# Kernel optimization log

Hardware: AMD Instinct MI355X
Metric: run time of the kernel (lower is better)

The kernel has to match this reference:

```python
import jax, jax.numpy as jnp
import numpy as np

B, N, C, D = 1, 8192, 256, 128
MASK_VAL = jnp.float32(-1e16)


def setup_inputs() -> dict:
    key = jax.random.key(0)
    k_in, k_g, k_w, k_b = jax.random.split(key, 4)
    inputs = jax.random.normal(k_in, (B, N, C), dtype=jnp.float32)
    # row has at least one unmasked entry (standard GAT practice).
    graph = (jax.random.uniform(k_g, (N, N)) < 0.01).astype(jnp.float32)
    graph = jnp.maximum(graph, jnp.eye(N, dtype=jnp.float32))
    W = jax.random.normal(k_w, (D, C), dtype=jnp.float32)  # nn.Linear weight [out,in]
    b = jax.random.normal(k_b, (D,), dtype=jnp.float32)
    return {"inputs": inputs, "graph": graph, "W": W, "b": b}


def reference(inputs, graph, W, b):
    # h = W(inputs): [B,N,D]
    h = jnp.einsum('bnc,dc->bnd', inputs, W)
    # dense scores masked by adjacency: [B,N,N]
    scores = jnp.einsum('bnd,bmd->bnm', h, h) * graph[None, :, :]
    # torch: masked_fill_(scores == 0, -1e16)
    scores = jnp.where(scores == 0.0, MASK_VAL, scores)
    attention = jax.nn.softmax(scores, axis=2)
    return jnp.einsum('bnm,bmd->bnd', attention, h) + b
```

## Files before the change

### kernel.cpp

```cpp
#include <hip/hip_runtime.h>
#include <math.h>

#define Nn 8192
#define Cc 256
#define Dd 128
#define CAP 192

typedef float fx4 __attribute__((ext_vector_type(4)));

__global__ __launch_bounds__(256) void wt_kernel(const float* __restrict__ W,
                                                 float4* __restrict__ WT) {
  const int t = blockIdx.x * 256 + threadIdx.x;
  const int c4 = t >> 7;
  const int d  = t & 127;
  const float4 v = *(const float4*)(W + (size_t)d * Cc + c4 * 4);
  WT[c4 * Dd + d] = v;
}

__global__ __launch_bounds__(256) void h_kernel(const float* __restrict__ x,
                                                const float4* __restrict__ WT,
                                                float* __restrict__ h) {
  const int tid = threadIdx.x;
  const int d = tid & 127;
  const int g = tid >> 7;
  const int r0 = blockIdx.x * 16 + g * 8;
  const float4* x4 = (const float4*)(x + (size_t)r0 * Cc);

  float acc[8];
#pragma unroll
  for (int r = 0; r < 8; ++r) acc[r] = 0.f;

#pragma unroll 4
  for (int c4 = 0; c4 < Cc / 4; ++c4) {
    const float4 w = WT[c4 * Dd + d];
#pragma unroll
    for (int r = 0; r < 8; ++r) {
      const float4 u = x4[r * (Cc / 4) + c4];
      acc[r] += u.x * w.x + u.y * w.y + u.z * w.z + u.w * w.w;
    }
  }
#pragma unroll
  for (int r = 0; r < 8; ++r) {
    h[(size_t)(r0 + r) * Dd + d] = acc[r];
  }
}

__global__ __launch_bounds__(256) void gat_fused(const float* __restrict__ graph,
                                                 const float* __restrict__ h,
                                                 const float* __restrict__ bias,
                                                 float* __restrict__ out) {
  __shared__ int idxs[4][CAP];
  const int wv   = threadIdx.x >> 6;
  const int lane = threadIdx.x & 63;
  const int i = blockIdx.x * 4 + wv;
  int* idx = idxs[wv];

  const float2 hi2 = *(const float2*)(h + (size_t)i * Dd + lane * 2);

  const fx4* row = (const fx4*)(graph + (size_t)i * Nn);
  const unsigned long long lmask = (1ull << lane) - 1ull;
  int cnt = 0;

  fx4 v[8];
#pragma unroll
  for (int t = 0; t < 8; ++t)
    v[t] = __builtin_nontemporal_load(&row[t * 64 + lane]);

#pragma unroll
  for (int c = 0; c < 4; ++c) {
    fx4 nv[8];
    if (c < 3) {
#pragma unroll
      for (int t = 0; t < 8; ++t)
        nv[t] = __builtin_nontemporal_load(&row[(c + 1) * 8 * 64 + t * 64 + lane]);
    }
#pragma unroll
    for (int t = 0; t < 8; ++t) {
      const int col = 4 * ((c * 8 + t) * 64 + lane);
      {
        const unsigned long long mk = __ballot(v[t].x != 0.f);
        const int p = cnt + __popcll(mk & lmask);
        if (v[t].x != 0.f && p < CAP) idx[p] = col + 0;
        cnt += __popcll(mk);
      }
      {
        const unsigned long long mk = __ballot(v[t].y != 0.f);
        const int p = cnt + __popcll(mk & lmask);
        if (v[t].y != 0.f && p < CAP) idx[p] = col + 1;
        cnt += __popcll(mk);
      }
      {
        const unsigned long long mk = __ballot(v[t].z != 0.f);
        const int p = cnt + __popcll(mk & lmask);
        if (v[t].z != 0.f && p < CAP) idx[p] = col + 2;
        cnt += __popcll(mk);
      }
      {
        const unsigned long long mk = __ballot(v[t].w != 0.f);
        const int p = cnt + __popcll(mk & lmask);
        if (v[t].w != 0.f && p < CAP) idx[p] = col + 3;
        cnt += __popcll(mk);
      }
    }
#pragma unroll
    for (int t = 0; t < 8; ++t) v[t] = nv[t];
  }
  const int m = min(cnt, CAP);

  float M = -INFINITY, L = 0.f;
  float accx = 0.f, accy = 0.f;

  float2 hv[8];
#pragma unroll
  for (int t = 0; t < 8; ++t) {
    if (t < m) {
      const int j = idx[t];
      hv[t] = *(const float2*)(h + (size_t)j * Dd + lane * 2);
    }
  }

  for (int e0 = 0; e0 < m; e0 += 8) {
    const int ne = min(8, m - e0);
    const int rem = m - e0 - 8;
    float2 nhv[8];
#pragma unroll
    for (int t = 0; t < 8; ++t) {
      if (t < rem) {
        const int j = idx[e0 + 8 + t];
        nhv[t] = *(const float2*)(h + (size_t)j * Dd + lane * 2);
      }
    }
#pragma unroll
    for (int t = 0; t < 8; ++t) {
      if (t < ne) {
        float pd = hi2.x * hv[t].x + hi2.y * hv[t].y;
#pragma unroll
        for (int off = 32; off > 0; off >>= 1) pd += __shfl_xor(pd, off);
        const float s = pd;
        if (s != 0.f) {
          const float newM = fmaxf(M, s);
          const float scale = __expf(M - newM);
          const float p = __expf(s - newM);
          L = L * scale + p;
          accx = accx * scale + p * hv[t].x;
          accy = accy * scale + p * hv[t].y;
          M = newM;
        }
      }
    }
#pragma unroll
    for (int t = 0; t < 8; ++t) hv[t] = nhv[t];
  }

  const float inv = 1.f / L;
  const float2 bv = *(const float2*)(bias + lane * 2);
  float2 o;
  o.x = accx * inv + bv.x;
  o.y = accy * inv + bv.y;
  *(float2*)(out + (size_t)i * Dd + lane * 2) = o;
}

extern "C" void kernel_launch(void* const* d_in, const int* in_sizes, int n_in,
                              void* d_out, int out_size, void* d_ws, size_t ws_size,
                              hipStream_t stream) {
  const float* x     = (const float*)d_in[0];
  const float* graph = (const float*)d_in[1];
  const float* W     = (const float*)d_in[2];
  const float* bias  = (const float*)d_in[3];
  float* out = (float*)d_out;

  float*  h  = (float*)d_ws;
  float4* WT = (float4*)((char*)d_ws + (16u << 20));

  wt_kernel<<<32, 256, 0, stream>>>(W, WT);
  h_kernel<<<Nn / 16, 256, 0, stream>>>(x, WT, h);
  gat_fused<<<Nn / 4, 256, 0, stream>>>(graph, h, bias, out);
}
```

Measured before the change: 459.3 us.

## Split wavefront into four 16-lane groups processing neighbors in parallel

The neighbor aggregation phase now splits each 64-lane wavefront into four 16-lane quarters. Each quarter handles a different neighbor and each lane holds 8 feature elements. This cuts the dot-product shuffle reduction from 6 steps to 4 and processes four edges per step instead of one. Each quarter keeps its own online-softmax state, and the four states are merged with cross-quarter shuffles at the end. This adds merge overhead and more registers per lane.

```diff
diff --git a/kernel.cpp b/kernel.cpp
--- a/kernel.cpp
+++ b/kernel.cpp
@@ -52,10 +52,13 @@
   __shared__ int idxs[4][CAP];
   const int wv   = threadIdx.x >> 6;
   const int lane = threadIdx.x & 63;
+  const int q    = lane >> 4;
+  const int ql   = lane & 15;
   const int i = blockIdx.x * 4 + wv;
   int* idx = idxs[wv];
 
-  const float2 hi2 = *(const float2*)(h + (size_t)i * Dd + lane * 2);
+  const float4 hiA = *(const float4*)(h + (size_t)i * Dd + ql * 8);
+  const float4 hiB = *(const float4*)(h + (size_t)i * Dd + ql * 8 + 4);
 
   const fx4* row = (const fx4*)(graph + (size_t)i * Nn);
   const unsigned long long lmask = (1ull << lane) - 1ull;
@@ -108,56 +111,97 @@
   const int m = min(cnt, CAP);
 
   float M = -INFINITY, L = 0.f;
-  float accx = 0.f, accy = 0.f;
-
-  float2 hv[8];
-#pragma unroll
-  for (int t = 0; t < 8; ++t) {
-    if (t < m) {
-      const int j = idx[t];
-      hv[t] = *(const float2*)(h + (size_t)j * Dd + lane * 2);
-    }
-  }
-
-  for (int e0 = 0; e0 < m; e0 += 8) {
-    const int ne = min(8, m - e0);
-    const int rem = m - e0 - 8;
-    float2 nhv[8];
-#pragma unroll
-    for (int t = 0; t < 8; ++t) {
-      if (t < rem) {
-        const int j = idx[e0 + 8 + t];
-        nhv[t] = *(const float2*)(h + (size_t)j * Dd + lane * 2);
-      }
-    }
-#pragma unroll
-    for (int t = 0; t < 8; ++t) {
-      if (t < ne) {
-        float pd = hi2.x * hv[t].x + hi2.y * hv[t].y;
-#pragma unroll
-        for (int off = 32; off > 0; off >>= 1) pd += __shfl_xor(pd, off);
-        const float s = pd;
-        if (s != 0.f) {
-          const float newM = fmaxf(M, s);
-          const float scale = __expf(M - newM);
-          const float p = __expf(s - newM);
-          L = L * scale + p;
-          accx = accx * scale + p * hv[t].x;
-          accy = accy * scale + p * hv[t].y;
-          M = newM;
-        }
-      }
-    }
-#pragma unroll
-    for (int t = 0; t < 8; ++t) hv[t] = nhv[t];
-  }
-
+  float4 accA = {0.f, 0.f, 0.f, 0.f};
+  float4 accB = {0.f, 0.f, 0.f, 0.f};
+
+  const int nsteps = (m + 3) >> 2;
+  const int nb = (nsteps + 1) >> 1;
+
+  float4 hvA[2], hvB[2];
+#pragma unroll
+  for (int u = 0; u < 2; ++u) {
+    const int e = u * 4 + q;
+    const int j = (e < m) ? idx[e] : i;
+    hvA[u] = *(const float4*)(h + (size_t)j * Dd + ql * 8);
+    hvB[u] = *(const float4*)(h + (size_t)j * Dd + ql * 8 + 4);
+  }
+
+  for (int b = 0; b < nb; ++b) {
+    float4 nA[2], nB[2];
+    if (b + 1 < nb) {
+#pragma unroll
+      for (int u = 0; u < 2; ++u) {
+        const int e = (2 * (b + 1) + u) * 4 + q;
+        const int j = (e < m) ? idx[e] : i;
+        nA[u] = *(const float4*)(h + (size_t)j * Dd + ql * 8);
+        nB[u] = *(const float4*)(h + (size_t)j * Dd + ql * 8 + 4);
+      }
+    }
+    float sv[2];
+#pragma unroll
+    for (int u = 0; u < 2; ++u) {
+      float pd = hiA.x * hvA[u].x + hiA.y * hvA[u].y + hiA.z * hvA[u].z + hiA.w * hvA[u].w
+               + hiB.x * hvB[u].x + hiB.y * hvB[u].y + hiB.z * hvB[u].z + hiB.w * hvB[u].w;
+#pragma unroll
+      for (int off = 8; off > 0; off >>= 1) pd += __shfl_xor(pd, off);
+      sv[u] = pd;
+    }
+#pragma unroll
+    for (int u = 0; u < 2; ++u) {
+      const int e = (2 * b + u) * 4 + q;
+      const float s = (e < m) ? sv[u] : 0.f;
+      if (s != 0.f) {
+        const float newM = fmaxf(M, s);
+        const float scale = __expf(M - newM);
+        const float p = __expf(s - newM);
+        L = L * scale + p;
+        accA.x = accA.x * scale + p * hvA[u].x;
+        accA.y = accA.y * scale + p * hvA[u].y;
+        accA.z = accA.z * scale + p * hvA[u].z;
+        accA.w = accA.w * scale + p * hvA[u].w;
+        accB.x = accB.x * scale + p * hvB[u].x;
+        accB.y = accB.y * scale + p * hvB[u].y;
+        accB.z = accB.z * scale + p * hvB[u].z;
+        accB.w = accB.w * scale + p * hvB[u].w;
+        M = newM;
+      }
+    }
+#pragma unroll
+    for (int u = 0; u < 2; ++u) { hvA[u] = nA[u]; hvB[u] = nB[u]; }
+  }
+
+#pragma unroll
+  for (int off = 16; off <= 32; off <<= 1) {
+    const float Mo = __shfl_xor(M, off);
+    const float Lo = __shfl_xor(L, off);
+    float4 aAo, aBo;
+    aAo.x = __shfl_xor(accA.x, off); aAo.y = __shfl_xor(accA.y, off);
+    aAo.z = __shfl_xor(accA.z, off); aAo.w = __shfl_xor(accA.w, off);
+    aBo.x = __shfl_xor(accB.x, off); aBo.y = __shfl_xor(accB.y, off);
+    aBo.z = __shfl_xor(accB.z, off); aBo.w = __shfl_xor(accB.w, off);
+    const float Mm = fmaxf(M, Mo);
+    const float s0 = (M  > -INFINITY) ? __expf(M  - Mm) : 0.f;
+    const float s1 = (Mo > -INFINITY) ? __expf(Mo - Mm) : 0.f;
+    L = L * s0 + Lo * s1;
+    accA.x = accA.x * s0 + aAo.x * s1;  accA.y = accA.y * s0 + aAo.y * s1;
+    accA.z = accA.z * s0 + aAo.z * s1;  accA.w = accA.w * s0 + aAo.w * s1;
+    accB.x = accB.x * s0 + aBo.x * s1;  accB.y = accB.y * s0 + aBo.y * s1;
+    accB.z = accB.z * s0 + aBo.z * s1;  accB.w = accB.w * s0 + aBo.w * s1;
+    M = Mm;
+  }
   const float inv = 1.f / L;
-  const float2 bv = *(const float2*)(bias + lane * 2);
-  float2 o;
-  o.x = accx * inv + bv.x;
-  o.y = accy * inv + bv.y;
-  *(float2*)(out + (size_t)i * Dd + lane * 2) = o;
+
+  if (q == 0) {
+    const float4 bA = *(const float4*)(bias + ql * 8);
+    const float4 bB = *(const float4*)(bias + ql * 8 + 4);
+    float4 oA, oB;
+    oA.x = accA.x * inv + bA.x;  oA.y = accA.y * inv + bA.y;
+    oA.z = accA.z * inv + bA.z;  oA.w = accA.w * inv + bA.w;
+    oB.x = accB.x * inv + bB.x;  oB.y = accB.y * inv + bB.y;
+    oB.z = accB.z * inv + bB.z;  oB.w = accB.w * inv + bB.w;
+    *(float4*)(out + (size_t)i * Dd + ql * 8)     = oA;
+    *(float4*)(out + (size_t)i * Dd + ql * 8 + 4) = oB;
+  }
 }
 
 extern "C" void kernel_launch(void* const* d_in, const int* in_sizes, int n_in,
```

Result: faster. 406.2 us (-11.6%).
